# Optimization experiments

Hardware: AMD Instinct MI355X
Metric: run time of the kernel (lower is better)

## Reference

```python
import jax, jax.numpy as jnp
import numpy as np


def setup_inputs() -> dict:
    key = jax.random.key(0)
    k1, k2, k3 = jax.random.split(key, 3)
    N1, N2, P, D = 4, 8, 1024, 128  # P = PH*PW = 32*32 (512px / 16 patch)
    feats = jax.random.normal(k1, (N1, P, D), dtype=jnp.float32)
    nfeats = jax.random.normal(k2, (N2, P, D), dtype=jnp.float32)
    background_masks = jax.random.uniform(k3, (N1, P), dtype=jnp.float32)
    return {"feats": feats, "nfeats": nfeats, "background_masks": background_masks,
            "PH": 32, "PW": 32, "H": 512, "W": 512}


def reference(feats, nfeats, background_masks, PH, PW, H, W):
    # L2-normalize patch embeddings (as in `f / f.norm(dim=-1, keepdim=True)`)
    f = feats / jnp.linalg.norm(feats, axis=-1, keepdims=True)    # [N1,P,D]
    g = nfeats / jnp.linalg.norm(nfeats, axis=-1, keepdims=True)  # [N2,Q,D]
    # Euclidean cdist of unit vectors: d^2 = 2 - 2*dot (clamped at 0)
    dot = jnp.einsum('npd,mqd->nmpq', f, g)                        # [N1,N2,P,Q]
    dist = jnp.sqrt(jnp.maximum(2.0 - 2.0 * dot, 0.0)) / 2.0      # cdist/2, permuted
    # min over normal patches Q -> per-query-patch nearest-neighbor distance
    scores_patch = dist.min(axis=-1)                               # [N1,N2,P]
    scores_patch = scores_patch * background_masks[:, None, :]
    # image score: max over query patches, mean over normal images
    scores = scores_patch.max(axis=-1).mean(axis=-1)               # [N1]
    # pixel map: mean over normal images, reshape to patch grid, bilinear upsample
    sp = scores_patch.mean(axis=1).reshape(-1, PH, PW)             # [N1,PH,PW]
    scores_pixel = jax.image.resize(sp, (sp.shape[0], H, W), method='bilinear')
    return scores, scores_pixel
```

## Files before the change

kernel.cpp:

```cpp
#include <hip/hip_runtime.h>

typedef __attribute__((ext_vector_type(8))) short short8;
typedef __attribute__((ext_vector_type(4))) float f32x4;
typedef __attribute__((ext_vector_type(4))) unsigned int u32x4;

static __device__ inline unsigned short f2bf(float x) {
    unsigned int u = __float_as_uint(x);
    u = (u + 0x7FFFu + ((u >> 16) & 1u)) >> 16;
    return (unsigned short)u;
}

static __device__ inline unsigned int pk(float a, float b, float inv) {
    return (unsigned int)f2bf(a * inv) | ((unsigned int)f2bf(b * inv) << 16);
}

__global__ __launch_bounds__(256, 2) void kscore(const float* __restrict__ feats,
                                                 const float* __restrict__ nfeats,
                                                 float* __restrict__ sp_part) {
    __shared__ char gtile[256 * 256];
    const int tid = threadIdx.x;
    const int lane = tid & 63;
    const int wave = tid >> 6;
    const int l15 = lane & 15, lhi = lane >> 4;
    const int m = blockIdx.x;
    const int ptile = blockIdx.y >> 2, qq = blockIdx.y & 3;
    const int rowbase = ptile * 256 + wave * 64;

    const float* gBase = nfeats + ((size_t)m * 1024 + qq * 256) * 128;

    short8 a[4][4];
    #pragma unroll
    for (int pg = 0; pg < 4; pg++) {
        const float* arow = feats + (size_t)(rowbase + pg * 16 + l15) * 128 + lhi * 8;
        f32x4 vx[4], vy[4];
        float ss = 0.f;
        #pragma unroll
        for (int kk = 0; kk < 4; kk++) {
            vx[kk] = *(const f32x4*)(arow + kk * 32);
            vy[kk] = *(const f32x4*)(arow + kk * 32 + 4);
            #pragma unroll
            for (int j = 0; j < 4; j++) ss += vx[kk][j]*vx[kk][j] + vy[kk][j]*vy[kk][j];
        }
        ss += __shfl_xor(ss, 16);
        ss += __shfl_xor(ss, 32);
        float inv = 1.0f / sqrtf(ss);
        #pragma unroll
        for (int kk = 0; kk < 4; kk++) {
            u32x4 o;
            o.x = pk(vx[kk][0], vx[kk][1], inv);
            o.y = pk(vx[kk][2], vx[kk][3], inv);
            o.z = pk(vy[kk][0], vy[kk][1], inv);
            o.w = pk(vy[kk][2], vy[kk][3], inv);
            a[pg][kk] = *(short8*)&o;
        }
    }

    {
        const int s0 = tid & 15;
        const int rb = tid >> 4;
        #pragma unroll
        for (int b = 0; b < 16; b++) {
            const int r = rb + b * 16;
            const float* src = gBase + (size_t)r * 128 + s0 * 8;
            f32x4 x = *(const f32x4*)(src);
            f32x4 y = *(const f32x4*)(src + 4);
            float ss = x[0]*x[0] + x[1]*x[1] + x[2]*x[2] + x[3]*x[3]
                     + y[0]*y[0] + y[1]*y[1] + y[2]*y[2] + y[3]*y[3];
            ss += __shfl_xor(ss, 1);
            ss += __shfl_xor(ss, 2);
            ss += __shfl_xor(ss, 4);
            ss += __shfl_xor(ss, 8);
            float inv = 1.0f / sqrtf(ss);
            u32x4 o;
            o.x = pk(x[0], x[1], inv);
            o.y = pk(x[2], x[3], inv);
            o.z = pk(y[0], y[1], inv);
            o.w = pk(y[2], y[3], inv);
            *(u32x4*)(gtile + ((r * 256 + s0 * 16) ^ ((r & 7) << 4))) = o;
        }
    }

    __syncthreads();

    f32x4 mx[4];
    #pragma unroll
    for (int pg = 0; pg < 4; pg++)
        #pragma unroll
        for (int i = 0; i < 4; i++) mx[pg][i] = -1e30f;

    #pragma unroll
    for (int qt = 0; qt < 16; qt++) {
        const int r = qt * 16 + l15;
        const int rowoff = r * 256;
        const int swz = (r & 7) << 4;
        short8 b0 = *(const short8*)(gtile + ((rowoff +   0 + lhi * 16) ^ swz));
        short8 b1 = *(const short8*)(gtile + ((rowoff +  64 + lhi * 16) ^ swz));
        short8 b2 = *(const short8*)(gtile + ((rowoff + 128 + lhi * 16) ^ swz));
        short8 b3 = *(const short8*)(gtile + ((rowoff + 192 + lhi * 16) ^ swz));
        f32x4 acc[4];
        #pragma unroll
        for (int pg = 0; pg < 4; pg++) {
            #pragma unroll
            for (int i = 0; i < 4; i++) acc[pg][i] = 0.f;
            acc[pg] = __builtin_amdgcn_mfma_f32_16x16x32_bf16(a[pg][0], b0, acc[pg], 0, 0, 0);
            acc[pg] = __builtin_amdgcn_mfma_f32_16x16x32_bf16(a[pg][1], b1, acc[pg], 0, 0, 0);
            acc[pg] = __builtin_amdgcn_mfma_f32_16x16x32_bf16(a[pg][2], b2, acc[pg], 0, 0, 0);
            acc[pg] = __builtin_amdgcn_mfma_f32_16x16x32_bf16(a[pg][3], b3, acc[pg], 0, 0, 0);
        }
        #pragma unroll
        for (int pg = 0; pg < 4; pg++)
            #pragma unroll
            for (int i = 0; i < 4; i++) mx[pg][i] = fmaxf(mx[pg][i], acc[pg][i]);
    }

    #pragma unroll
    for (int pg = 0; pg < 4; pg++)
        #pragma unroll
        for (int i = 0; i < 4; i++) {
            float v = mx[pg][i];
            v = fmaxf(v, __shfl_xor(v, 1));
            v = fmaxf(v, __shfl_xor(v, 2));
            v = fmaxf(v, __shfl_xor(v, 4));
            v = fmaxf(v, __shfl_xor(v, 8));
            mx[pg][i] = v;
        }
    if (l15 == 0) {
        #pragma unroll
        for (int pg = 0; pg < 4; pg++)
            #pragma unroll
            for (int i = 0; i < 4; i++) {
                int row = rowbase + pg * 16 + lhi * 4 + i;
                int n = row >> 10, p = row & 1023;
                sp_part[((size_t)(n * 8 + m) * 4 + qq) * 1024 + p] = mx[pg][i];
            }
    }
}

__global__ __launch_bounds__(256) void kfinal(const float* __restrict__ sp_part,
                                              const float* __restrict__ mask,
                                              float* __restrict__ out) {
    const int n = blockIdx.y;
    const int bx = blockIdx.x;
    const int t = threadIdx.x;
    float* pix = out + 4;

    if (bx == 64) {
        __shared__ float smax[4];
        float acc = 0.f;
        for (int m = 0; m < 8; m++) {
            const float* base = sp_part + (size_t)(n * 8 + m) * 4 * 1024;
            float lm = -1e30f;
            #pragma unroll
            for (int i = 0; i < 4; i++) {
                int p = i * 256 + t;
                float dot = fmaxf(fmaxf(base[p], base[1024 + p]),
                                  fmaxf(base[2048 + p], base[3072 + p]));
                float d = sqrtf(fmaxf(2.0f - 2.0f * dot, 0.0f)) * 0.5f * mask[n * 1024 + p];
                lm = fmaxf(lm, d);
            }
            #pragma unroll
            for (int d = 32; d; d >>= 1) lm = fmaxf(lm, __shfl_xor(lm, d));
            if ((t & 63) == 0) smax[t >> 6] = lm;
            __syncthreads();
            if (t == 0) acc += fmaxf(fmaxf(smax[0], smax[1]), fmaxf(smax[2], smax[3]));
            __syncthreads();
        }
        if (t == 0) out[n] = acc * 0.125f;
        return;
    }

    __shared__ float sp_row[2][32];
    const int band = bx * 8;
    const int pr_lo = (int)floorf((band + 0.5f) * 0.0625f - 0.5f);
    const int row0 = min(max(pr_lo, 0), 31);
    const int row1 = min(max(pr_lo + 1, 0), 31);
    {
        int v = t >> 2, sub = t & 3;
        int vr = v >> 5, vc = v & 31;
        int p = (vr ? row1 : row0) * 32 + vc;
        float sum = 0.f;
        #pragma unroll
        for (int mi = 0; mi < 2; mi++) {
            int m = sub * 2 + mi;
            const float* base = sp_part + (size_t)(n * 8 + m) * 4 * 1024 + p;
            float dot = fmaxf(fmaxf(base[0], base[1024]),
                              fmaxf(base[2048], base[3072]));
            sum += sqrtf(fmaxf(2.0f - 2.0f * dot, 0.0f)) * 0.5f;
        }
        sum *= mask[n * 1024 + p];
        sum += __shfl_xor(sum, 1);
        sum += __shfl_xor(sum, 2);
        if (sub == 0) sp_row[vr][vc] = sum * 0.125f;
    }
    __syncthreads();
    #pragma unroll
    for (int i = 0; i < 16; i++) {
        int idx = i * 256 + t;
        int yl = idx >> 9, x = idx & 511;
        int y = band + yl;
        float fy = (y + 0.5f) * 0.0625f - 0.5f;
        float ty = fy - (float)pr_lo;
        float fx = (x + 0.5f) * 0.0625f - 0.5f;
        float xf = floorf(fx);
        float tx = fx - xf;
        int x0 = (int)xf;
        int x0c = min(max(x0, 0), 31), x1c = min(max(x0 + 1, 0), 31);
        float v00 = sp_row[0][x0c], v01 = sp_row[0][x1c];
        float v10 = sp_row[1][x0c], v11 = sp_row[1][x1c];
        float v0 = v00 + tx * (v01 - v00);
        float v1 = v10 + tx * (v11 - v10);
        pix[(size_t)n * 262144 + (size_t)y * 512 + x] = v0 + ty * (v1 - v0);
    }
}

extern "C" void kernel_launch(void* const* d_in, const int* in_sizes, int n_in,
                              void* d_out, int out_size, void* d_ws, size_t ws_size,
                              hipStream_t stream) {
    const float* feats = (const float*)d_in[0];
    const float* nfeats = (const float*)d_in[1];
    const float* mask = (const float*)d_in[2];
    float* out = (float*)d_out;

    float* sp_part = (float*)d_ws;

    kscore<<<dim3(8, 64), 256, 0, stream>>>(feats, nfeats, sp_part);
    kfinal<<<dim3(65, 4), 256, 0, stream>>>(sp_part, mask, out);
}
```

Baseline: 34.87 us.

## Precompute row norms in separate kernel, halve Q tile, use hardware bf16 convert

Adds a small pre-pass kernel that computes inverse L2 norms for every feats and nfeats row. Previously each score block recomputed the norms of its 256 query rows redundantly. The score kernel now splits Q into 8 chunks of 128 instead of 4 of 256. This halves LDS use, doubles the grid to 1024 blocks and raises the occupancy hint to 4. Software bf16 rounding is replaced with the v_cvt_pk_bf16_f32 instruction, at the cost of an extra launch and twice as many partial maxima for the final kernel to reduce.

```diff
diff --git a/kernel.cpp b/kernel.cpp
--- a/kernel.cpp
+++ b/kernel.cpp
@@ -4,53 +4,59 @@
 typedef __attribute__((ext_vector_type(4))) float f32x4;
 typedef __attribute__((ext_vector_type(4))) unsigned int u32x4;
 
-static __device__ inline unsigned short f2bf(float x) {
-    unsigned int u = __float_as_uint(x);
-    u = (u + 0x7FFFu + ((u >> 16) & 1u)) >> 16;
-    return (unsigned short)u;
-}
-
-static __device__ inline unsigned int pk(float a, float b, float inv) {
-    return (unsigned int)f2bf(a * inv) | ((unsigned int)f2bf(b * inv) << 16);
-}
-
-__global__ __launch_bounds__(256, 2) void kscore(const float* __restrict__ feats,
+static __device__ inline unsigned int cvtpk(float a, float b) {
+    unsigned int r;
+    asm("v_cvt_pk_bf16_f32 %0, %1, %2" : "=v"(r) : "v"(a), "v"(b));
+    return r;
+}
+
+__global__ __launch_bounds__(256) void knormv(const float* __restrict__ feats,
+                                              const float* __restrict__ nfeats,
+                                              float* __restrict__ invn) {
+    int row = blockIdx.x * 16 + (threadIdx.x >> 4);
+    int s = threadIdx.x & 15;
+    const float* src = (row < 4096) ? feats + (size_t)row * 128
+                                    : nfeats + (size_t)(row - 4096) * 128;
+    f32x4 x = *(const f32x4*)(src + s * 8);
+    f32x4 y = *(const f32x4*)(src + s * 8 + 4);
+    float ss = x[0]*x[0] + x[1]*x[1] + x[2]*x[2] + x[3]*x[3]
+             + y[0]*y[0] + y[1]*y[1] + y[2]*y[2] + y[3]*y[3];
+    ss += __shfl_xor(ss, 1);
+    ss += __shfl_xor(ss, 2);
+    ss += __shfl_xor(ss, 4);
+    ss += __shfl_xor(ss, 8);
+    if (s == 0) invn[row] = 1.0f / sqrtf(ss);
+}
+
+__global__ __launch_bounds__(256, 4) void kscore(const float* __restrict__ feats,
                                                  const float* __restrict__ nfeats,
+                                                 const float* __restrict__ invn,
                                                  float* __restrict__ sp_part) {
-    __shared__ char gtile[256 * 256];
+    __shared__ char gtile[128 * 256];
     const int tid = threadIdx.x;
     const int lane = tid & 63;
     const int wave = tid >> 6;
     const int l15 = lane & 15, lhi = lane >> 4;
     const int m = blockIdx.x;
-    const int ptile = blockIdx.y >> 2, qq = blockIdx.y & 3;
+    const int ptile = blockIdx.y >> 3, qq = blockIdx.y & 7;
     const int rowbase = ptile * 256 + wave * 64;
-
-    const float* gBase = nfeats + ((size_t)m * 1024 + qq * 256) * 128;
+    const int gRow0 = m * 1024 + qq * 128;
 
     short8 a[4][4];
     #pragma unroll
     for (int pg = 0; pg < 4; pg++) {
-        const float* arow = feats + (size_t)(rowbase + pg * 16 + l15) * 128 + lhi * 8;
-        f32x4 vx[4], vy[4];
-        float ss = 0.f;
+        const int row = rowbase + pg * 16 + l15;
+        const float inv = invn[row];
+        const float* arow = feats + (size_t)row * 128 + lhi * 8;
         #pragma unroll
         for (int kk = 0; kk < 4; kk++) {
-            vx[kk] = *(const f32x4*)(arow + kk * 32);
-            vy[kk] = *(const f32x4*)(arow + kk * 32 + 4);
-            #pragma unroll
-            for (int j = 0; j < 4; j++) ss += vx[kk][j]*vx[kk][j] + vy[kk][j]*vy[kk][j];
-        }
-        ss += __shfl_xor(ss, 16);
-        ss += __shfl_xor(ss, 32);
-        float inv = 1.0f / sqrtf(ss);
-        #pragma unroll
-        for (int kk = 0; kk < 4; kk++) {
+            f32x4 x = *(const f32x4*)(arow + kk * 32);
+            f32x4 y = *(const f32x4*)(arow + kk * 32 + 4);
             u32x4 o;
-            o.x = pk(vx[kk][0], vx[kk][1], inv);
-            o.y = pk(vx[kk][2], vx[kk][3], inv);
-            o.z = pk(vy[kk][0], vy[kk][1], inv);
-            o.w = pk(vy[kk][2], vy[kk][3], inv);
+            o.x = cvtpk(x[0] * inv, x[1] * inv);
+            o.y = cvtpk(x[2] * inv, x[3] * inv);
+            o.z = cvtpk(y[0] * inv, y[1] * inv);
+            o.w = cvtpk(y[2] * inv, y[3] * inv);
             a[pg][kk] = *(short8*)&o;
         }
     }
@@ -59,23 +65,17 @@
         const int s0 = tid & 15;
         const int rb = tid >> 4;
         #pragma unroll
-        for (int b = 0; b < 16; b++) {
+        for (int b = 0; b < 8; b++) {
             const int r = rb + b * 16;
-            const float* src = gBase + (size_t)r * 128 + s0 * 8;
+            const float inv = invn[4096 + gRow0 + r];
+            const float* src = nfeats + (size_t)(gRow0 + r) * 128 + s0 * 8;
             f32x4 x = *(const f32x4*)(src);
             f32x4 y = *(const f32x4*)(src + 4);
-            float ss = x[0]*x[0] + x[1]*x[1] + x[2]*x[2] + x[3]*x[3]
-                     + y[0]*y[0] + y[1]*y[1] + y[2]*y[2] + y[3]*y[3];
-            ss += __shfl_xor(ss, 1);
-            ss += __shfl_xor(ss, 2);
-            ss += __shfl_xor(ss, 4);
-            ss += __shfl_xor(ss, 8);
-            float inv = 1.0f / sqrtf(ss);
             u32x4 o;
-            o.x = pk(x[0], x[1], inv);
-            o.y = pk(x[2], x[3], inv);
-            o.z = pk(y[0], y[1], inv);
-            o.w = pk(y[2], y[3], inv);
+            o.x = cvtpk(x[0] * inv, x[1] * inv);
+            o.y = cvtpk(x[2] * inv, x[3] * inv);
+            o.z = cvtpk(y[0] * inv, y[1] * inv);
+            o.w = cvtpk(y[2] * inv, y[3] * inv);
             *(u32x4*)(gtile + ((r * 256 + s0 * 16) ^ ((r & 7) << 4))) = o;
         }
     }
@@ -89,7 +89,7 @@
         for (int i = 0; i < 4; i++) mx[pg][i] = -1e30f;
 
     #pragma unroll
-    for (int qt = 0; qt < 16; qt++) {
+    for (int qt = 0; qt < 8; qt++) {
         const int r = qt * 16 + l15;
         const int rowoff = r * 256;
         const int swz = (r & 7) << 4;
@@ -131,7 +131,7 @@
             for (int i = 0; i < 4; i++) {
                 int row = rowbase + pg * 16 + lhi * 4 + i;
                 int n = row >> 10, p = row & 1023;
-                sp_part[((size_t)(n * 8 + m) * 4 + qq) * 1024 + p] = mx[pg][i];
+                sp_part[((size_t)(n * 8 + m) * 8 + qq) * 1024 + p] = mx[pg][i];
             }
     }
 }
@@ -148,13 +148,14 @@
         __shared__ float smax[4];
         float acc = 0.f;
         for (int m = 0; m < 8; m++) {
-            const float* base = sp_part + (size_t)(n * 8 + m) * 4 * 1024;
+            const float* base = sp_part + (size_t)(n * 8 + m) * 8 * 1024;
             float lm = -1e30f;
             #pragma unroll
             for (int i = 0; i < 4; i++) {
                 int p = i * 256 + t;
-                float dot = fmaxf(fmaxf(base[p], base[1024 + p]),
-                                  fmaxf(base[2048 + p], base[3072 + p]));
+                float dot = -1e30f;
+                #pragma unroll
+                for (int s = 0; s < 8; s++) dot = fmaxf(dot, base[s * 1024 + p]);
                 float d = sqrtf(fmaxf(2.0f - 2.0f * dot, 0.0f)) * 0.5f * mask[n * 1024 + p];
                 lm = fmaxf(lm, d);
             }
@@ -182,9 +183,10 @@
         #pragma unroll
         for (int mi = 0; mi < 2; mi++) {
             int m = sub * 2 + mi;
-            const float* base = sp_part + (size_t)(n * 8 + m) * 4 * 1024 + p;
-            float dot = fmaxf(fmaxf(base[0], base[1024]),
-                              fmaxf(base[2048], base[3072]));
+            const float* base = sp_part + (size_t)(n * 8 + m) * 8 * 1024 + p;
+            float dot = -1e30f;
+            #pragma unroll
+            for (int s = 0; s < 8; s++) dot = fmaxf(dot, base[s * 1024]);
             sum += sqrtf(fmaxf(2.0f - 2.0f * dot, 0.0f)) * 0.5f;
         }
         sum *= mask[n * 1024 + p];
@@ -221,8 +223,10 @@
     const float* mask = (const float*)d_in[2];
     float* out = (float*)d_out;
 
-    float* sp_part = (float*)d_ws;
-
-    kscore<<<dim3(8, 64), 256, 0, stream>>>(feats, nfeats, sp_part);
+    float* invn = (float*)d_ws;
+    float* sp_part = (float*)((char*)d_ws + 65536);
+
+    knormv<<<768, 256, 0, stream>>>(feats, nfeats, invn);
+    kscore<<<dim3(8, 128), 256, 0, stream>>>(feats, nfeats, invn, sp_part);
     kfinal<<<dim3(65, 4), 256, 0, stream>>>(sp_part, mask, out);
 }
```

Result: slower. 45.52 us (+30.6%).
